# Performance work log

Measured on AMD Instinct MI355X. Metric: run time of the kernel, lower is better.

## Reference

```python
import math
import jax, jax.numpy as jnp
import numpy as np

MIN_AMT, MAX_AMT = 1, 32
C = 3
B, H, W = 128, 224, 224


def build_kernel_table():
    # kernels[i] has size = i + MIN_AMT: vertical center column, each channel sums to 1,
    # zero-padded (centered) to MAX_AMT x MAX_AMT (pad_to_width).
    tbl = np.zeros((MAX_AMT - MIN_AMT + 1, MAX_AMT, MAX_AMT, C), np.float32)
    for i, size in enumerate(range(MIN_AMT, MAX_AMT + 1)):
        pad = MAX_AMT - size
        t = pad // 2
        col = t + size // 2
        tbl[i, t:t + size, col, :] = 1.0 / size
    return jnp.asarray(tbl)


def setup_inputs() -> dict:
    key = jax.random.key(0)
    k1, k2, k3 = jax.random.split(key, 3)
    x = jax.random.uniform(k1, (B, H, W, C), jnp.float32)  # image batch
    amt = jax.random.randint(k2, (B,), MIN_AMT, MAX_AMT, dtype=jnp.int32)  # [min, max)
    angles = jax.random.randint(k3, (B,), 0, 91, dtype=jnp.int32)  # degrees [0, 91)
    return {"x": x, "kernels_table": build_kernel_table(), "amt": amt, "angles": angles}


def _rotate_nearest(img, rad):
    # img: (K, K, C); nearest-neighbor rotation about image center (tf.contrib.image.rotate
    # convention: output (x,y) samples input at [cos -sin; sin cos] @ (x,y) + centering offset).
    K = img.shape[0]
    cos, sin = jnp.cos(rad), jnp.sin(rad)
    coords = jnp.arange(K, dtype=jnp.float32)
    yy, xx = jnp.meshgrid(coords, coords, indexing="ij")
    e = jnp.float32(K - 1)
    x_off = (e - (cos * e - sin * e)) * 0.5
    y_off = (e - (sin * e + cos * e)) * 0.5
    sx = cos * xx - sin * yy + x_off
    sy = sin * xx + cos * yy + y_off
    ix = jnp.round(sx).astype(jnp.int32)
    iy = jnp.round(sy).astype(jnp.int32)
    valid = (ix >= 0) & (ix < K) & (iy >= 0) & (iy < K)
    g = img[jnp.clip(iy, 0, K - 1), jnp.clip(ix, 0, K - 1)]  # (K, K, C)
    return jnp.where(valid[..., None], g, jnp.float32(0.0))


def _depthwise_conv(img, ker):
    # img: (H, W, C); ker: (K, K, C) -> per-channel SAME conv, stride 1.
    out = jax.lax.conv_general_dilated(
        img[None], ker[:, :, None, :], (1, 1), "SAME",
        dimension_numbers=("NHWC", "HWIO", "NHWC"), feature_group_count=C)
    return out[0]


def reference(x, kernels_table, amt, angles):
    ker = kernels_table[amt]                                # (B, K, K, C) per-sample gather
    rad = angles.astype(jnp.float32) * jnp.float32(math.pi / 180.0)
    ker = jax.vmap(_rotate_nearest)(ker, rad)               # per-sample rotation
    out = jax.vmap(_depthwise_conv)(x, ker)                 # per-sample depthwise conv
    return out.reshape(-1, 224, 224, 3)
```

## Files before the change

kernel.cpp:

```cpp
#include <hip/hip_runtime.h>
#include <math.h>

namespace {

constexpr int Himg = 224, Wimg = 224, Cn = 3, Kk = 32;
constexpr int MAXT = 64;
constexpr int WSTRIDE = 512;
constexpr int IMG_F  = Himg * Wimg * Cn;
constexpr int ROW_F  = Wimg * Cn;
constexpr int ROW_B  = ROW_F * 4;

constexpr int IN_CH  = 144;
constexpr int ED_CH  = 24;
constexpr int IN_PER_IMG = Himg * IN_CH;
constexpr int ED_PER_IMG = Himg * ED_CH;
constexpr int IN_BLK = IN_PER_IMG / 256;
constexpr int ED_BLK = ED_PER_IMG / 256;
constexpr int BLK_PER_IMG = IN_BLK + ED_BLK;
constexpr int FAST_LO = 9, FAST_HI = 117;

typedef float v4  __attribute__((ext_vector_type(4), aligned(4)));
typedef float v4a __attribute__((ext_vector_type(4), aligned(16)));


__global__ __launch_bounds__(64)
void build_taps(const float* __restrict__ tbl,
                const int* __restrict__ amt,
                const int* __restrict__ ang,
                int* __restrict__ ws)
{
    const int b   = blockIdx.x;
    const int tid = threadIdx.x;

    __shared__ int   s_cnt;
    __shared__ float s_w;
    __shared__ int   s_dky[MAXT], s_dkx[MAXT];

    if (tid == 0) { s_cnt = 0; s_w = 0.0f; }
    __syncthreads();

    const int a = amt[b];
    const float  rad = (float)ang[b] * (float)(M_PI / 180.0);
    const double rd  = (double)rad;
    const float  cth = (float)cos(rd);
    const float  sth = (float)sin(rd);
    const float  e   = 31.0f;
    const float xoff = __fmul_rn(__fsub_rn(e, __fsub_rn(__fmul_rn(cth, e), __fmul_rn(sth, e))), 0.5f);
    const float yoff = __fmul_rn(__fsub_rn(e, __fadd_rn(__fmul_rn(sth, e), __fmul_rn(cth, e))), 0.5f);

    for (int p = tid; p < Kk * Kk; p += 64) {
        const int   ky = p >> 5, kx = p & 31;
        const float xf = (float)kx, yf = (float)ky;
        const float sx = __fadd_rn(__fsub_rn(__fmul_rn(cth, xf), __fmul_rn(sth, yf)), xoff);
        const float sy = __fadd_rn(__fadd_rn(__fmul_rn(sth, xf), __fmul_rn(cth, yf)), yoff);
        const int ix = (int)rintf(sx);
        const int iy = (int)rintf(sy);
        if (ix >= 0 && ix < Kk && iy >= 0 && iy < Kk) {
            const float v = tbl[((a * Kk + iy) * Kk + ix) * Cn];
            if (v != 0.0f) {
                const int idx = atomicAdd(&s_cnt, 1);
                if (idx < MAXT) {
                    s_dky[idx] = ky - 15;
                    s_dkx[idx] = kx - 15;
                    s_w = v;
                }
            }
        }
    }
    __syncthreads();

    const int n = min(s_cnt, MAXT);
    int* wsb = ws + b * WSTRIDE;
    if (tid == 0) { wsb[0] = n; wsb[1] = __float_as_int(s_w); }
    for (int i = tid; i < n; i += 64) {
        wsb[2 + i]   = s_dky[i];
        wsb[66 + i]  = s_dkx[i];
        wsb[130 + i] = s_dky[i] * ROW_B + s_dkx[i] * (int)(Cn * sizeof(float));
    }
}

__global__ __launch_bounds__(256)
void blur_direct(const float* __restrict__ x,
                 const int* __restrict__ ws,
                 float* __restrict__ out,
                 int B)
{
    const int tid = threadIdx.x;
    const int L   = blockIdx.x;

    int b, c;
    if (B == 128) {
        const int xcd = L & 7;
        const int j   = L >> 3;
        const int g   = j / BLK_PER_IMG;
        c = j - g * BLK_PER_IMG;
        b = g * 8 + xcd;
    } else {
        b = L / BLK_PER_IMG;
        c = L - b * BLK_PER_IMG;
    }

    __shared__ int shNW[2];
    __shared__ int s_dky[MAXT], s_dkx[MAXT], s_xoff[MAXT];
    const int* wsb = ws + b * WSTRIDE;
    if (tid < 2)    shNW[tid]   = wsb[tid];
    if (tid < MAXT) {
        s_dky[tid]  = wsb[2 + tid];
        s_dkx[tid]  = wsb[66 + tid];
        s_xoff[tid] = wsb[130 + tid];
    }
    __syncthreads();

    const int   n = shNW[0];
    const float w = __int_as_float(shNW[1]);
    const float* xb = x + (size_t)b * IMG_F;

    if (c < IN_BLK) {
        const int ii = c * 256 + tid;
        const int y  = ii / IN_CH;
        const int k  = ii - y * IN_CH + 12;
        const int fbase = y * ROW_F + 4 * k;
        const char* base = (const char*)xb + (size_t)fbase * 4;

        float a0 = 0.0f, a1 = 0.0f, a2 = 0.0f, a3 = 0.0f;

        if (c >= FAST_LO && c < FAST_HI) {
            int i = 0;
            for (; i + 4 <= n; i += 4) {
                const v4 f0 = *(const v4*)(base + s_xoff[i]);
                const v4 f1 = *(const v4*)(base + s_xoff[i + 1]);
                const v4 f2 = *(const v4*)(base + s_xoff[i + 2]);
                const v4 f3 = *(const v4*)(base + s_xoff[i + 3]);
                a0 += f0.x; a1 += f0.y; a2 += f0.z; a3 += f0.w;
                a0 += f1.x; a1 += f1.y; a2 += f1.z; a3 += f1.w;
                a0 += f2.x; a1 += f2.y; a2 += f2.z; a3 += f2.w;
                a0 += f3.x; a1 += f3.y; a2 += f3.z; a3 += f3.w;
            }
            for (; i < n; ++i) {
                const v4 f = *(const v4*)(base + s_xoff[i]);
                a0 += f.x; a1 += f.y; a2 += f.z; a3 += f.w;
            }
        } else {
            for (int i = 0; i < n; ++i) {
                const int  row = y + s_dky[i];
                const bool ok  = (unsigned)row < (unsigned)Himg;
                const int  off = ok ? s_xoff[i] : 0;
                const float m  = ok ? 1.0f : 0.0f;
                const v4 f = *(const v4*)(base + off);
                a0 += m * f.x; a1 += m * f.y; a2 += m * f.z; a3 += m * f.w;
            }
        }

        float* o = out + (size_t)b * IMG_F + fbase;
        __builtin_nontemporal_store(v4a{a0 * w, a1 * w, a2 * w, a3 * w}, (v4a*)o);
    } else {
        const int ee = (c - IN_BLK) * 256 + tid;
        const int y  = ee / ED_CH;
        const int j  = ee - y * ED_CH;
        const int k  = (j < 12) ? j : (j + 144);
        const int fd0 = 4 * k;

        float acc[4] = {0.0f, 0.0f, 0.0f, 0.0f};
        for (int i = 0; i < n; ++i) {
            const int  row = y + s_dky[i];
            const bool rok = (unsigned)row < (unsigned)Himg;
            const int  s0  = fd0 + 3 * s_dkx[i];
            const int  ob  = row * ROW_F + s0;
#pragma unroll
            for (int q = 0; q < 4; ++q) {
                const bool ok  = rok & ((unsigned)(s0 + q) < (unsigned)ROW_F);
                const int  off = ok ? (ob + q) : 0;
                const float v  = xb[off];
                acc[q] += ok ? v : 0.0f;
            }
        }

        float* o = out + (size_t)b * IMG_F + (size_t)y * ROW_F + fd0;
        __builtin_nontemporal_store(
            v4a{acc[0] * w, acc[1] * w, acc[2] * w, acc[3] * w}, (v4a*)o);
    }
}

}

extern "C" void kernel_launch(void* const* d_in, const int* in_sizes, int n_in,
                              void* d_out, int out_size, void* d_ws, size_t ws_size,
                              hipStream_t stream) {
    const float* x   = (const float*)d_in[0];
    const float* tbl = (const float*)d_in[1];
    const int*   amt = (const int*)d_in[2];
    const int*   ang = (const int*)d_in[3];
    float*       out = (float*)d_out;
    int*         ws  = (int*)d_ws;

    const int B = in_sizes[2];

    build_taps<<<B, 64, 0, stream>>>(tbl, amt, ang, ws);
    blur_direct<<<B * BLK_PER_IMG, 256, 0, stream>>>(x, ws, out, B);
}
```

Baseline: 228.5 us.

## Register-block four output rows per thread in blur kernel

Each thread now computes four consecutive output rows for its column slot, reusing the per-tap offset read from shared memory and issuing four independent vector loads per tap. The grid shrinks about fourfold and launch bounds request two blocks per SIMD. This amortizes index and tap overhead and raises memory-level parallelism, at the cost of more registers and fewer blocks to hide latency. The fast/slow boundary split is moved to row-group granularity.

```diff
diff --git a/kernel.cpp b/kernel.cpp
--- a/kernel.cpp
+++ b/kernel.cpp
@@ -12,12 +12,12 @@
 
 constexpr int IN_CH  = 144;
 constexpr int ED_CH  = 24;
-constexpr int IN_PER_IMG = Himg * IN_CH;
-constexpr int ED_PER_IMG = Himg * ED_CH;
-constexpr int IN_BLK = IN_PER_IMG / 256;
-constexpr int ED_BLK = ED_PER_IMG / 256;
+constexpr int YG     = Himg / 4;
+constexpr int IN_IT  = YG * IN_CH;
+constexpr int ED_IT  = YG * ED_CH;
+constexpr int IN_BLK = (IN_IT + 255) / 256;
+constexpr int ED_BLK = (ED_IT + 255) / 256;
 constexpr int BLK_PER_IMG = IN_BLK + ED_BLK;
-constexpr int FAST_LO = 9, FAST_HI = 117;
 
 typedef float v4  __attribute__((ext_vector_type(4), aligned(4)));
 typedef float v4a __attribute__((ext_vector_type(4), aligned(16)));
@@ -79,11 +79,11 @@
     }
 }
 
-__global__ __launch_bounds__(256)
-void blur_direct(const float* __restrict__ x,
-                 const int* __restrict__ ws,
-                 float* __restrict__ out,
-                 int B)
+__global__ __launch_bounds__(256, 2)
+void blur_rb4(const float* __restrict__ x,
+              const int* __restrict__ ws,
+              float* __restrict__ out,
+              int B)
 {
     const int tid = threadIdx.x;
     const int L   = blockIdx.x;
@@ -116,68 +116,85 @@
     const float* xb = x + (size_t)b * IMG_F;
 
     if (c < IN_BLK) {
-        const int ii = c * 256 + tid;
-        const int y  = ii / IN_CH;
-        const int k  = ii - y * IN_CH + 12;
-        const int fbase = y * ROW_F + 4 * k;
+        const int idx = c * 256 + tid;
+        if (idx >= IN_IT) return;
+        const int y4 = idx / IN_CH;
+        const int kk = idx - y4 * IN_CH;
+        const int k  = kk + 12;
+        const int y0 = y4 * 4;
+        const int fbase = y0 * ROW_F + 4 * k;
         const char* base = (const char*)xb + (size_t)fbase * 4;
 
-        float a0 = 0.0f, a1 = 0.0f, a2 = 0.0f, a3 = 0.0f;
-
-        if (c >= FAST_LO && c < FAST_HI) {
-            int i = 0;
-            for (; i + 4 <= n; i += 4) {
-                const v4 f0 = *(const v4*)(base + s_xoff[i]);
-                const v4 f1 = *(const v4*)(base + s_xoff[i + 1]);
-                const v4 f2 = *(const v4*)(base + s_xoff[i + 2]);
-                const v4 f3 = *(const v4*)(base + s_xoff[i + 3]);
-                a0 += f0.x; a1 += f0.y; a2 += f0.z; a3 += f0.w;
-                a0 += f1.x; a1 += f1.y; a2 += f1.z; a3 += f1.w;
-                a0 += f2.x; a1 += f2.y; a2 += f2.z; a3 += f2.w;
-                a0 += f3.x; a1 += f3.y; a2 += f3.z; a3 += f3.w;
-            }
-            for (; i < n; ++i) {
-                const v4 f = *(const v4*)(base + s_xoff[i]);
-                a0 += f.x; a1 += f.y; a2 += f.z; a3 += f.w;
+        v4 acc0 = {0,0,0,0}, acc1 = {0,0,0,0}, acc2 = {0,0,0,0}, acc3 = {0,0,0,0};
+
+        if (y4 >= 4 && y4 < 52) {
+            for (int i = 0; i < n; ++i) {
+                const int off = s_xoff[i];
+                const v4 f0 = *(const v4*)(base + off);
+                const v4 f1 = *(const v4*)(base + off + ROW_B);
+                const v4 f2 = *(const v4*)(base + off + 2 * ROW_B);
+                const v4 f3 = *(const v4*)(base + off + 3 * ROW_B);
+                acc0 += f0; acc1 += f1; acc2 += f2; acc3 += f3;
             }
         } else {
             for (int i = 0; i < n; ++i) {
-                const int  row = y + s_dky[i];
-                const bool ok  = (unsigned)row < (unsigned)Himg;
-                const int  off = ok ? s_xoff[i] : 0;
-                const float m  = ok ? 1.0f : 0.0f;
-                const v4 f = *(const v4*)(base + off);
-                a0 += m * f.x; a1 += m * f.y; a2 += m * f.z; a3 += m * f.w;
+                const int off = s_xoff[i];
+                const int r0  = y0 + s_dky[i];
+                const bool ok0 = (unsigned)(r0)     < (unsigned)Himg;
+                const bool ok1 = (unsigned)(r0 + 1) < (unsigned)Himg;
+                const bool ok2 = (unsigned)(r0 + 2) < (unsigned)Himg;
+                const bool ok3 = (unsigned)(r0 + 3) < (unsigned)Himg;
+                const v4 f0 = *(const v4*)(base + (ok0 ? off             : 0));
+                const v4 f1 = *(const v4*)(base + (ok1 ? off +     ROW_B : 0));
+                const v4 f2 = *(const v4*)(base + (ok2 ? off + 2 * ROW_B : 0));
+                const v4 f3 = *(const v4*)(base + (ok3 ? off + 3 * ROW_B : 0));
+                const float m0 = ok0 ? 1.0f : 0.0f;
+                const float m1 = ok1 ? 1.0f : 0.0f;
+                const float m2 = ok2 ? 1.0f : 0.0f;
+                const float m3 = ok3 ? 1.0f : 0.0f;
+                acc0 += m0 * f0; acc1 += m1 * f1; acc2 += m2 * f2; acc3 += m3 * f3;
             }
         }
 
         float* o = out + (size_t)b * IMG_F + fbase;
-        __builtin_nontemporal_store(v4a{a0 * w, a1 * w, a2 * w, a3 * w}, (v4a*)o);
+        __builtin_nontemporal_store(v4a{acc0.x * w, acc0.y * w, acc0.z * w, acc0.w * w}, (v4a*)o);
+        __builtin_nontemporal_store(v4a{acc1.x * w, acc1.y * w, acc1.z * w, acc1.w * w}, (v4a*)(o + ROW_F));
+        __builtin_nontemporal_store(v4a{acc2.x * w, acc2.y * w, acc2.z * w, acc2.w * w}, (v4a*)(o + 2 * ROW_F));
+        __builtin_nontemporal_store(v4a{acc3.x * w, acc3.y * w, acc3.z * w, acc3.w * w}, (v4a*)(o + 3 * ROW_F));
     } else {
-        const int ee = (c - IN_BLK) * 256 + tid;
-        const int y  = ee / ED_CH;
-        const int j  = ee - y * ED_CH;
+        const int e = (c - IN_BLK) * 256 + tid;
+        if (e >= ED_IT) return;
+        const int y4 = e / ED_CH;
+        const int j  = e - y4 * ED_CH;
         const int k  = (j < 12) ? j : (j + 144);
         const int fd0 = 4 * k;
-
-        float acc[4] = {0.0f, 0.0f, 0.0f, 0.0f};
+        const int y0  = 4 * y4;
+
+        float acc[4][4] = {};
         for (int i = 0; i < n; ++i) {
-            const int  row = y + s_dky[i];
-            const bool rok = (unsigned)row < (unsigned)Himg;
-            const int  s0  = fd0 + 3 * s_dkx[i];
-            const int  ob  = row * ROW_F + s0;
+            const int s0 = fd0 + 3 * s_dkx[i];
+            const int r0 = y0 + s_dky[i];
 #pragma unroll
             for (int q = 0; q < 4; ++q) {
-                const bool ok  = rok & ((unsigned)(s0 + q) < (unsigned)ROW_F);
-                const int  off = ok ? (ob + q) : 0;
-                const float v  = xb[off];
-                acc[q] += ok ? v : 0.0f;
-            }
-        }
-
-        float* o = out + (size_t)b * IMG_F + (size_t)y * ROW_F + fd0;
-        __builtin_nontemporal_store(
-            v4a{acc[0] * w, acc[1] * w, acc[2] * w, acc[3] * w}, (v4a*)o);
+                const int  row = r0 + q;
+                const bool rok = (unsigned)row < (unsigned)Himg;
+                const int  ob  = row * ROW_F + s0;
+#pragma unroll
+                for (int ch = 0; ch < 4; ++ch) {
+                    const bool ok  = rok & ((unsigned)(s0 + ch) < (unsigned)ROW_F);
+                    const float v = xb[ok ? (ob + ch) : 0];
+                    acc[q][ch] += ok ? v : 0.0f;
+                }
+            }
+        }
+
+        float* o = out + (size_t)b * IMG_F + (size_t)y0 * ROW_F + fd0;
+#pragma unroll
+        for (int q = 0; q < 4; ++q) {
+            __builtin_nontemporal_store(
+                v4a{acc[q][0] * w, acc[q][1] * w, acc[q][2] * w, acc[q][3] * w},
+                (v4a*)(o + q * ROW_F));
+        }
     }
 }
 
@@ -196,5 +213,5 @@
     const int B = in_sizes[2];
 
     build_taps<<<B, 64, 0, stream>>>(tbl, amt, ang, ws);
-    blur_direct<<<B * BLK_PER_IMG, 256, 0, stream>>>(x, ws, out, B);
-}
+    blur_rb4<<<B * BLK_PER_IMG, 256, 0, stream>>>(x, ws, out, B);
+}
```

Measured after the change: 259.5 us. 1.14x slower.

## Stage halo tiles in LDS and accumulate taps from shared memory

Applied to the files above, without the earlier changes.

Replaces the direct global-memory gather blur with a tiled kernel. Each block loads a 32-row by 56-float4 output tile plus a 31-row and 48-float halo into LDS, zero-padded so no bounds checks are needed. All taps are then accumulated from shared memory, with misalignment handled by four shift cases. This is meant to cut redundant global and L2 reads across taps, at the cost of a large halo load per tile (about 80 KB of LDS per block, so roughly two blocks per CU) and double LDS reads on unaligned taps.

```diff
diff --git a/kernel.cpp b/kernel.cpp
--- a/kernel.cpp
+++ b/kernel.cpp
@@ -10,14 +10,15 @@
 constexpr int ROW_F  = Wimg * Cn;
 constexpr int ROW_B  = ROW_F * 4;
 
-constexpr int IN_CH  = 144;
-constexpr int ED_CH  = 24;
-constexpr int IN_PER_IMG = Himg * IN_CH;
-constexpr int ED_PER_IMG = Himg * ED_CH;
-constexpr int IN_BLK = IN_PER_IMG / 256;
-constexpr int ED_BLK = ED_PER_IMG / 256;
-constexpr int BLK_PER_IMG = IN_BLK + ED_BLK;
-constexpr int FAST_LO = 9, FAST_HI = 117;
+constexpr int TW = 56;
+constexpr int TH = 32;
+constexpr int TILES_X = 3;
+constexpr int TILES_Y = 7;
+constexpr int TPI = TILES_X * TILES_Y;
+constexpr int L_W = 320;
+constexpr int L_H = TH + 31;
+constexpr int L_SZ = L_W * L_H;
+constexpr int OUT_PT = (TW * TH) / 256;
 
 typedef float v4  __attribute__((ext_vector_type(4), aligned(4)));
 typedef float v4a __attribute__((ext_vector_type(4), aligned(16)));
@@ -79,105 +80,119 @@
     }
 }
 
-__global__ __launch_bounds__(256)
-void blur_direct(const float* __restrict__ x,
-                 const int* __restrict__ ws,
-                 float* __restrict__ out,
-                 int B)
+__global__ __launch_bounds__(256, 2)
+void blur_lds(const float* __restrict__ x,
+              const int* __restrict__ ws,
+              float* __restrict__ out,
+              int B)
 {
     const int tid = threadIdx.x;
     const int L   = blockIdx.x;
 
-    int b, c;
+    int b, t;
     if (B == 128) {
         const int xcd = L & 7;
         const int j   = L >> 3;
-        const int g   = j / BLK_PER_IMG;
-        c = j - g * BLK_PER_IMG;
+        const int g   = j / TPI;
+        t = j - g * TPI;
         b = g * 8 + xcd;
     } else {
-        b = L / BLK_PER_IMG;
-        c = L - b * BLK_PER_IMG;
-    }
-
-    __shared__ int shNW[2];
-    __shared__ int s_dky[MAXT], s_dkx[MAXT], s_xoff[MAXT];
+        b = L / TPI;
+        t = L - b * TPI;
+    }
+    const int ty = t / TILES_X;
+    const int tx = t - ty * TILES_X;
+    const int y0 = ty * TH;
+    const int k0 = tx * TW;
+    const int g0 = 4 * k0 - 48;
+    const int r0 = y0 - 15;
+
+    __shared__ float lds[L_SZ];
+    __shared__ int   shNW[2];
+    __shared__ int   s_dky[MAXT], s_dkx[MAXT];
+
     const int* wsb = ws + b * WSTRIDE;
-    if (tid < 2)    shNW[tid]   = wsb[tid];
+    if (tid < 2)    shNW[tid]  = wsb[tid];
     if (tid < MAXT) {
-        s_dky[tid]  = wsb[2 + tid];
-        s_dkx[tid]  = wsb[66 + tid];
-        s_xoff[tid] = wsb[130 + tid];
+        s_dky[tid] = wsb[2 + tid];
+        s_dkx[tid] = wsb[66 + tid];
+    }
+
+    const float* xb = x + (size_t)b * IMG_F;
+    for (int u = tid; u < L_H * 80; u += 256) {
+        const int lr  = u / 80;
+        const int lc4 = (u - lr * 80) * 4;
+        const int gr  = r0 + lr;
+        const int gc  = g0 + lc4;
+        v4 val = {0.0f, 0.0f, 0.0f, 0.0f};
+        if ((unsigned)gr < (unsigned)Himg && (unsigned)gc < (unsigned)ROW_F)
+            val = *(const v4a*)(xb + (size_t)gr * ROW_F + gc);
+        *(v4a*)(&lds[lr * L_W + lc4]) = val;
     }
     __syncthreads();
 
     const int   n = shNW[0];
     const float w = __int_as_float(shNW[1]);
-    const float* xb = x + (size_t)b * IMG_F;
-
-    if (c < IN_BLK) {
-        const int ii = c * 256 + tid;
-        const int y  = ii / IN_CH;
-        const int k  = ii - y * IN_CH + 12;
-        const int fbase = y * ROW_F + 4 * k;
-        const char* base = (const char*)xb + (size_t)fbase * 4;
-
-        float a0 = 0.0f, a1 = 0.0f, a2 = 0.0f, a3 = 0.0f;
-
-        if (c >= FAST_LO && c < FAST_HI) {
-            int i = 0;
-            for (; i + 4 <= n; i += 4) {
-                const v4 f0 = *(const v4*)(base + s_xoff[i]);
-                const v4 f1 = *(const v4*)(base + s_xoff[i + 1]);
-                const v4 f2 = *(const v4*)(base + s_xoff[i + 2]);
-                const v4 f3 = *(const v4*)(base + s_xoff[i + 3]);
-                a0 += f0.x; a1 += f0.y; a2 += f0.z; a3 += f0.w;
-                a0 += f1.x; a1 += f1.y; a2 += f1.z; a3 += f1.w;
-                a0 += f2.x; a1 += f2.y; a2 += f2.z; a3 += f2.w;
-                a0 += f3.x; a1 += f3.y; a2 += f3.z; a3 += f3.w;
-            }
-            for (; i < n; ++i) {
-                const v4 f = *(const v4*)(base + s_xoff[i]);
-                a0 += f.x; a1 += f.y; a2 += f.z; a3 += f.w;
+
+    int lbase[OUT_PT];
+#pragma unroll
+    for (int p = 0; p < OUT_PT; ++p) {
+        const int o = tid + 256 * p;
+        const int r = o / TW;
+        const int c = o - r * TW;
+        lbase[p] = (r + 15) * L_W + 4 * c + 48;
+    }
+
+    v4 acc[OUT_PT];
+#pragma unroll
+    for (int p = 0; p < OUT_PT; ++p) acc[p] = v4{0.0f, 0.0f, 0.0f, 0.0f};
+
+    for (int i = 0; i < n; ++i) {
+        const int dky  = __builtin_amdgcn_readfirstlane(s_dky[i]);
+        const int dkx  = __builtin_amdgcn_readfirstlane(s_dkx[i]);
+        const int toff = dky * L_W + 3 * dkx;
+        const int s    = toff & 3;
+        const int ta   = toff - s;
+
+        if (s == 0) {
+#pragma unroll
+            for (int p = 0; p < OUT_PT; ++p) {
+                const v4 f = *(const v4a*)(&lds[lbase[p] + ta]);
+                acc[p].x += f.x; acc[p].y += f.y; acc[p].z += f.z; acc[p].w += f.w;
+            }
+        } else if (s == 1) {
+#pragma unroll
+            for (int p = 0; p < OUT_PT; ++p) {
+                const v4 A = *(const v4a*)(&lds[lbase[p] + ta]);
+                const v4 Bv = *(const v4a*)(&lds[lbase[p] + ta + 4]);
+                acc[p].x += A.y; acc[p].y += A.z; acc[p].z += A.w; acc[p].w += Bv.x;
+            }
+        } else if (s == 2) {
+#pragma unroll
+            for (int p = 0; p < OUT_PT; ++p) {
+                const v4 A = *(const v4a*)(&lds[lbase[p] + ta]);
+                const v4 Bv = *(const v4a*)(&lds[lbase[p] + ta + 4]);
+                acc[p].x += A.z; acc[p].y += A.w; acc[p].z += Bv.x; acc[p].w += Bv.y;
             }
         } else {
-            for (int i = 0; i < n; ++i) {
-                const int  row = y + s_dky[i];
-                const bool ok  = (unsigned)row < (unsigned)Himg;
-                const int  off = ok ? s_xoff[i] : 0;
-                const float m  = ok ? 1.0f : 0.0f;
-                const v4 f = *(const v4*)(base + off);
-                a0 += m * f.x; a1 += m * f.y; a2 += m * f.z; a3 += m * f.w;
+#pragma unroll
+            for (int p = 0; p < OUT_PT; ++p) {
+                const v4 A = *(const v4a*)(&lds[lbase[p] + ta]);
+                const v4 Bv = *(const v4a*)(&lds[lbase[p] + ta + 4]);
+                acc[p].x += A.w; acc[p].y += Bv.x; acc[p].z += Bv.y; acc[p].w += Bv.z;
             }
         }
-
-        float* o = out + (size_t)b * IMG_F + fbase;
-        __builtin_nontemporal_store(v4a{a0 * w, a1 * w, a2 * w, a3 * w}, (v4a*)o);
-    } else {
-        const int ee = (c - IN_BLK) * 256 + tid;
-        const int y  = ee / ED_CH;
-        const int j  = ee - y * ED_CH;
-        const int k  = (j < 12) ? j : (j + 144);
-        const int fd0 = 4 * k;
-
-        float acc[4] = {0.0f, 0.0f, 0.0f, 0.0f};
-        for (int i = 0; i < n; ++i) {
-            const int  row = y + s_dky[i];
-            const bool rok = (unsigned)row < (unsigned)Himg;
-            const int  s0  = fd0 + 3 * s_dkx[i];
-            const int  ob  = row * ROW_F + s0;
-#pragma unroll
-            for (int q = 0; q < 4; ++q) {
-                const bool ok  = rok & ((unsigned)(s0 + q) < (unsigned)ROW_F);
-                const int  off = ok ? (ob + q) : 0;
-                const float v  = xb[off];
-                acc[q] += ok ? v : 0.0f;
-            }
-        }
-
-        float* o = out + (size_t)b * IMG_F + (size_t)y * ROW_F + fd0;
+    }
+
+    float* ob = out + (size_t)b * IMG_F + (size_t)y0 * ROW_F + 4 * k0;
+#pragma unroll
+    for (int p = 0; p < OUT_PT; ++p) {
+        const int o = tid + 256 * p;
+        const int r = o / TW;
+        const int c = o - r * TW;
         __builtin_nontemporal_store(
-            v4a{acc[0] * w, acc[1] * w, acc[2] * w, acc[3] * w}, (v4a*)o);
+            v4a{acc[p].x * w, acc[p].y * w, acc[p].z * w, acc[p].w * w},
+            (v4a*)(ob + r * ROW_F + 4 * c));
     }
 }
 
@@ -196,5 +211,5 @@
     const int B = in_sizes[2];
 
     build_taps<<<B, 64, 0, stream>>>(tbl, amt, ang, ws);
-    blur_direct<<<B * BLK_PER_IMG, 256, 0, stream>>>(x, ws, out, B);
-}
+    blur_lds<<<B * TPI, 256, 0, stream>>>(x, ws, out, B);
+}
```

Result: slower. 286.3 us (+25.3%).
